# Optimization experiments

Hardware: AMD Instinct MI355X
Metric: run time of the kernel (lower is better)

Reference implementation:

```python
import jax, jax.numpy as jnp
import numpy as np
from jax import lax

N, T, U, V = 32, 512, 100, 4096
BLANK = 0


def setup_inputs() -> dict:
    key = jax.random.key(0)
    k1, k2, k3, k4, k5 = jax.random.split(key, 5)
    encoder_out = jax.random.normal(k1, (N, T, V), dtype=jnp.float32)
    decoder_out = jax.random.normal(k2, (N, U + 1, V), dtype=jnp.float32)
    targets = jax.random.randint(k3, (N, U), 1, V)            # labels, never blank
    input_lengths = jax.random.randint(k4, (N,), T // 2, T + 1)
    target_lengths = jax.random.randint(k5, (N,), U // 2, U + 1)
    return {
        "encoder_out": encoder_out,
        "decoder_out": decoder_out,
        "targets": targets,
        "input_lengths": input_lengths,
        "target_lengths": target_lengths,
    }


def _logprob_single(enc, dec, y, in_len, tgt_len):
    # enc: (T, V)  dec: (U+1, V)  y: (U,)
    Um = y.shape[0]
    u_idx = jnp.arange(Um)
    # emit[t, u] = enc[t, y[u]] + dec[u, y[u]]  (cost of emitting label u+1 at time t)
    emit = enc[:, y] + dec[u_idx, y][None, :]          # (T, U)
    blank_e = enc[:, BLANK]                            # (T,)
    blank_d = dec[:, BLANK]                            # (U+1,)

    # t = 0 row: alpha[0, u] = sum_{k<u} emit[0, k]
    alpha0 = jnp.concatenate([jnp.zeros((1,), enc.dtype), jnp.cumsum(emit[0])])

    def row_step(alpha_prev, xs):
        be_prev, emit_t = xs
        # blank transition from row t-1 (same u)
        top = alpha_prev + be_prev + blank_d           # (U+1,)

        # label transition within row: alpha[u] = logaddexp(top[u], alpha[u-1] + emit_t[u-1])
        def u_step(carry, x):
            top_u, em = x
            a = jnp.logaddexp(top_u, carry + em)
            return a, a

        _, rest = lax.scan(u_step, top[0], (top[1:], emit_t))
        alpha = jnp.concatenate([top[:1], rest])
        return alpha, alpha

    _, rows = lax.scan(row_step, alpha0, (blank_e[:-1], emit[1:]))
    alphas = jnp.concatenate([alpha0[None, :], rows], axis=0)   # (T, U+1)

    # log p(y|x) = alpha[T-1, U] + enc[T-1, blank] + dec[U, blank] with true lengths
    return alphas[in_len - 1, tgt_len] + enc[in_len - 1, BLANK] + dec[tgt_len, BLANK]


def reference(encoder_out, decoder_out, targets, input_lengths, target_lengths):
    # reduction='none': returns per-utterance log p(y|x), shape (N,)
    return jax.vmap(_logprob_single)(encoder_out, decoder_out, targets,
                                     input_lengths, target_lengths)
```

## Files before the change

### kernel.cpp

```cpp
#include <hip/hip_runtime.h>

#define NB 32
#define TT 512
#define UU 100
#define UM 101
#define VV 4096
#define NEG (-1e30f)
#define WIN 64
#define L2E 1.4426950408889634f
#define LN2 0.6931471805599453f

__device__ __forceinline__ float vexp2(float x){ float r; asm("v_exp_f32 %0, %1" : "=v"(r) : "v"(x)); return r; }
__device__ __forceinline__ float vlog2(float x){ float r; asm("v_log_f32 %0, %1" : "=v"(r) : "v"(x)); return r; }

__device__ __forceinline__ float lae2(float a, float b) {
    float m  = fmaxf(a, b);
    float nd = fminf(a, b) - m;
    return m + vlog2(1.0f + vexp2(nd));
}

__global__ __launch_bounds__(1024, 1) void fused_k(
        const float* __restrict__ enc, const float* __restrict__ dec,
        const int* __restrict__ tgt, const int* __restrict__ ilen,
        const int* __restrict__ tlen, float* __restrict__ out) {
    __shared__ float em[2][WIN][128];
    __shared__ float blkL[864];
    __shared__ int   tgtL[UU];
    __shared__ float dvxL[UU];

    int n = blockIdx.x;
    int tid = threadIdx.x;
    int tin = ilen[n], tg = tlen[n];
    int dend = tin - 1 + tg;
    int E = (dend + WIN - 1) / WIN;
    const float* encn = enc + (size_t)n * TT * VV;

    for (int i = tid; i < 864; i += 1024)
        blkL[i] = (i >= 128 && i < 128 + TT) ? encn[(size_t)(i - 128) * VV] * L2E : NEG;
    if (tid < UU) {
        int y = tgt[n * UU + tid];
        tgtL[tid] = y;
        dvxL[tid] = dec[((size_t)n * UM + tid) * VV + y] * L2E;
    }
    __syncthreads();

    int wave = tid >> 6;
    int lane = tid & 63;

    auto FILLWIN = [&](int w, int baseDp) {
        int pid = tid - 64;
        float* emw = &em[w][0][0];
#pragma unroll
        for (int it = 0; it < 9; ++it) {
            int idx = pid + it * 960;
            if (idx < WIN * 128) {
                int dm = idx >> 7, u = idx & 127;
                int d = baseDp + dm + 1;
                int t = d - u;
                float val = NEG;
                if (u >= 1 && u <= tg && t >= 0 && t < tin)
                    val = fmaf(encn[(size_t)t * VV + tgtL[u - 1]], L2E, dvxL[u - 1]);
                emw[idx] = val;
            }
        }
    };

    if (wave != 0) FILLWIN(0, 0);

    int u0c = min(2 * lane, UM - 1), u1c = min(2 * lane + 1, UM - 1);
    float bd0 = dec[((size_t)n * UM + u0c) * VV] * L2E;
    float bd1 = dec[((size_t)n * UM + u1c) * VV] * L2E;
    int ib0 = 127 - 2 * lane;
    bool cap0 = (2 * lane == tg), cap1 = (2 * lane + 1 == tg);
    bool fx16 = (lane == 16), fx32 = (lane == 32), fx48 = (lane == 48);
    float a0 = (lane == 0) ? 0.0f : NEG;
    float a1 = NEG;
    float res = NEG;

    float Ae0[8], Ae1[8], Ab0[8], Ab1[8], Be0[8], Be1[8], Bb0[8], Bb1[8];

    auto REFILL = [&](float (&Re0)[8], float (&Re1)[8], float (&Rb0)[8], float (&Rb1)[8],
                      int j0, int dbase, const float* emb) {
#pragma unroll
        for (int k = 0; k < 8; ++k) {
            int dm = j0 + k;
            float2 ev = *(const float2*)(emb + dm * 128 + 2 * lane);
            int d = dbase + dm + 1;
            Re0[k] = ev.x; Re1[k] = ev.y;
            Rb0[k] = blkL[ib0 + d] + bd0;
            Rb1[k] = blkL[ib0 + d - 1] + bd1;
        }
        __builtin_amdgcn_sched_barrier(0);
    };

    auto STEPS = [&](float (&Re0)[8], float (&Re1)[8], float (&Rb0)[8], float (&Rb1)[8],
                     int j0, int dbase) {
#pragma unroll
        for (int k = 0; k < 8; ++k) {
            int dd = dbase + j0 + k + 1;
            int sh = __builtin_amdgcn_update_dpp(__float_as_int(NEG), __float_as_int(a1),
                                                 0x111, 0xF, 0xF, false);
            float s15 = __int_as_float(__builtin_amdgcn_readlane(__float_as_int(a1), 15));
            float s31 = __int_as_float(__builtin_amdgcn_readlane(__float_as_int(a1), 31));
            float s47 = __int_as_float(__builtin_amdgcn_readlane(__float_as_int(a1), 47));
            float l0 = __int_as_float(sh);
            l0 = fx16 ? s15 : l0;
            l0 = fx32 ? s31 : l0;
            l0 = fx48 ? s47 : l0;
            float bt0 = a0 + Rb0[k], et0 = l0 + Re0[k];
            float bt1 = a1 + Rb1[k], et1 = a0 + Re1[k];
            a0 = lae2(bt0, et0);
            a1 = lae2(bt1, et1);
            if (dd == dend) { if (cap0) res = a0; if (cap1) res = a1; }
        }
        __builtin_amdgcn_sched_barrier(0);
    };

    __syncthreads();

    for (int e = 0; e < E; ++e) {
        if (wave == 0) {
            int dbase = e * WIN;
            const float* emb = &em[e & 1][0][0];
            REFILL(Ae0, Ae1, Ab0, Ab1, 0, dbase, emb);
            REFILL(Be0, Be1, Bb0, Bb1, 8, dbase, emb);  STEPS(Ae0, Ae1, Ab0, Ab1, 0, dbase);
            REFILL(Ae0, Ae1, Ab0, Ab1, 16, dbase, emb); STEPS(Be0, Be1, Bb0, Bb1, 8, dbase);
            REFILL(Be0, Be1, Bb0, Bb1, 24, dbase, emb); STEPS(Ae0, Ae1, Ab0, Ab1, 16, dbase);
            REFILL(Ae0, Ae1, Ab0, Ab1, 32, dbase, emb); STEPS(Be0, Be1, Bb0, Bb1, 24, dbase);
            REFILL(Be0, Be1, Bb0, Bb1, 40, dbase, emb); STEPS(Ae0, Ae1, Ab0, Ab1, 32, dbase);
            REFILL(Ae0, Ae1, Ab0, Ab1, 48, dbase, emb); STEPS(Be0, Be1, Bb0, Bb1, 40, dbase);
            REFILL(Be0, Be1, Bb0, Bb1, 56, dbase, emb); STEPS(Ae0, Ae1, Ab0, Ab1, 48, dbase);
            STEPS(Be0, Be1, Bb0, Bb1, 56, dbase);
        } else {
            FILLWIN((e + 1) & 1, (e + 1) * WIN);
        }
        __syncthreads();
    }

    if (wave == 0 && (cap0 | cap1)) {
        float fin  = blkL[128 + tin - 1];
        float bdtg = dec[((size_t)n * UM + tg) * VV] * L2E;
        out[n] = (res + fin + bdtg) * LN2;
    }
}

extern "C" void kernel_launch(void* const* d_in, const int* in_sizes, int n_in,
                              void* d_out, int out_size, void* d_ws, size_t ws_size,
                              hipStream_t hs) {
    const float* enc  = (const float*)d_in[0];
    const float* dec  = (const float*)d_in[1];
    const int*   tgt  = (const int*)d_in[2];
    const int*   ilen = (const int*)d_in[3];
    const int*   tlen = (const int*)d_in[4];
    float* out = (float*)d_out;

    hipLaunchKernelGGL(fused_k, dim3(NB), dim3(1024), 0, hs,
                       enc, dec, tgt, ilen, tlen, out);
}
```

Before: 71.90 us.

## Replace block barriers with LDS ring buffer and flag-based producer/consumer sync

Swaps the double-buffered window plus __syncthreads handoff between the compute wave and the 15 loader waves for a 4-slot LDS ring. The slots are coordinated by per-slot completion counters and a consumer progress counter, with waits done by spinning and s_sleep. The window shrinks from 64 to 32 diagonals and the row pitch from 128 to 104, so loaders can run several windows ahead and the serial DP wave no longer stalls at block-wide barriers. The cost is spin-wait overhead and a dependence on LDS memory ordering through fences and atomics, which could hide subtle races.

New measurement: 71.81 us. No clear change (-0.1%).

```diff
diff --git a/kernel.cpp b/kernel.cpp
--- a/kernel.cpp
+++ b/kernel.cpp
@@ -6,7 +6,10 @@
 #define UM 101
 #define VV 4096
 #define NEG (-1e30f)
-#define WIN 64
+#define WIN 32
+#define RING 4
+#define PITCH 104
+#define EMSLOT (WIN * PITCH + 24)
 #define L2E 1.4426950408889634f
 #define LN2 0.6931471805599453f
 
@@ -23,53 +26,67 @@
         const float* __restrict__ enc, const float* __restrict__ dec,
         const int* __restrict__ tgt, const int* __restrict__ ilen,
         const int* __restrict__ tlen, float* __restrict__ out) {
-    __shared__ float em[2][WIN][128];
+    __shared__ float emL[RING][EMSLOT];
     __shared__ float blkL[864];
+    __shared__ float dvxL[UU];
     __shared__ int   tgtL[UU];
-    __shared__ float dvxL[UU];
+    __shared__ int   fin[RING];
+    __shared__ int   cons;
 
-    int n = blockIdx.x;
-    int tid = threadIdx.x;
+    int n = blockIdx.x, tid = threadIdx.x;
     int tin = ilen[n], tg = tlen[n];
     int dend = tin - 1 + tg;
     int E = (dend + WIN - 1) / WIN;
     const float* encn = enc + (size_t)n * TT * VV;
+    const float* decn = dec + (size_t)n * UM * VV;
 
     for (int i = tid; i < 864; i += 1024)
         blkL[i] = (i >= 128 && i < 128 + TT) ? encn[(size_t)(i - 128) * VV] * L2E : NEG;
     if (tid < UU) {
         int y = tgt[n * UU + tid];
         tgtL[tid] = y;
-        dvxL[tid] = dec[((size_t)n * UM + tid) * VV + y] * L2E;
+        dvxL[tid] = decn[(size_t)tid * VV + y] * L2E;
     }
+    if (tid < RING) fin[tid] = 0;
+    if (tid == RING) cons = 0;
     __syncthreads();
 
-    int wave = tid >> 6;
-    int lane = tid & 63;
+    int wave = tid >> 6, lane = tid & 63;
 
-    auto FILLWIN = [&](int w, int baseDp) {
-        int pid = tid - 64;
-        float* emw = &em[w][0][0];
+    if (wave != 0) {
+        int cbase = (wave - 1) * 64 + lane;
+        for (int w = 0; w < E; ++w) {
+            int s = w & (RING - 1);
+            while (*(volatile int*)&cons + RING <= w) __builtin_amdgcn_s_sleep(2);
+            float ev[4]; bool ok[4]; int dmA[4], uA[4];
 #pragma unroll
-        for (int it = 0; it < 9; ++it) {
-            int idx = pid + it * 960;
-            if (idx < WIN * 128) {
-                int dm = idx >> 7, u = idx & 127;
-                int d = baseDp + dm + 1;
-                int t = d - u;
-                float val = NEG;
-                if (u >= 1 && u <= tg && t >= 0 && t < tin)
-                    val = fmaf(encn[(size_t)t * VV + tgtL[u - 1]], L2E, dvxL[u - 1]);
-                emw[idx] = val;
+            for (int it = 0; it < 4; ++it) {
+                int c = cbase + it * 960;
+                int dm = (unsigned)c / PITCH;
+                int u  = c - dm * PITCH;
+                int d  = w * WIN + 1 + dm;
+                int t  = d - u;
+                bool v = (c < WIN * PITCH) & (u >= 1) & (u <= tg) & (t >= 0) & (t < tin);
+                dmA[it] = dm; uA[it] = u; ok[it] = v;
+                ev[it] = NEG;
+                if (v) ev[it] = encn[(size_t)t * VV + tgtL[u - 1]];
             }
+#pragma unroll
+            for (int it = 0; it < 4; ++it) {
+                int c = cbase + it * 960;
+                if (c < WIN * PITCH) {
+                    float e = ok[it] ? fmaf(ev[it], L2E, dvxL[uA[it] - 1]) : NEG;
+                    emL[s][dmA[it] * PITCH + uA[it]] = e;
+                }
+            }
+            __threadfence_block();
+            if (lane == 0) atomicAdd(&fin[s], 1);
         }
-    };
+        return;
+    }
 
-    if (wave != 0) FILLWIN(0, 0);
-
-    int u0c = min(2 * lane, UM - 1), u1c = min(2 * lane + 1, UM - 1);
-    float bd0 = dec[((size_t)n * UM + u0c) * VV] * L2E;
-    float bd1 = dec[((size_t)n * UM + u1c) * VV] * L2E;
+    float bd0 = decn[(size_t)min(2 * lane, UM - 1) * VV] * L2E;
+    float bd1 = decn[(size_t)min(2 * lane + 1, UM - 1) * VV] * L2E;
     int ib0 = 127 - 2 * lane;
     bool cap0 = (2 * lane == tg), cap1 = (2 * lane + 1 == tg);
     bool fx16 = (lane == 16), fx32 = (lane == 32), fx48 = (lane == 48);
@@ -79,25 +96,24 @@
 
     float Ae0[8], Ae1[8], Ab0[8], Ab1[8], Be0[8], Be1[8], Bb0[8], Bb1[8];
 
-    auto REFILL = [&](float (&Re0)[8], float (&Re1)[8], float (&Rb0)[8], float (&Rb1)[8],
-                      int j0, int dbase, const float* emb) {
+    auto REFILL = [&](float (&e0)[8], float (&e1)[8], float (&b0)[8], float (&b1)[8],
+                      const float* emb, int j0, int base) {
 #pragma unroll
         for (int k = 0; k < 8; ++k) {
-            int dm = j0 + k;
-            float2 ev = *(const float2*)(emb + dm * 128 + 2 * lane);
-            int d = dbase + dm + 1;
-            Re0[k] = ev.x; Re1[k] = ev.y;
-            Rb0[k] = blkL[ib0 + d] + bd0;
-            Rb1[k] = blkL[ib0 + d - 1] + bd1;
+            int dm = j0 + k, d = base + 1 + dm;
+            float2 ev = *(const float2*)(emb + dm * PITCH + 2 * lane);
+            e0[k] = ev.x; e1[k] = ev.y;
+            b0[k] = blkL[ib0 + d] + bd0;
+            b1[k] = blkL[ib0 + d - 1] + bd1;
         }
         __builtin_amdgcn_sched_barrier(0);
     };
 
-    auto STEPS = [&](float (&Re0)[8], float (&Re1)[8], float (&Rb0)[8], float (&Rb1)[8],
-                     int j0, int dbase) {
+    auto STEPS = [&](float (&e0)[8], float (&e1)[8], float (&b0)[8], float (&b1)[8],
+                     int j0, int base) {
 #pragma unroll
         for (int k = 0; k < 8; ++k) {
-            int dd = dbase + j0 + k + 1;
+            int dd = base + 1 + j0 + k;
             int sh = __builtin_amdgcn_update_dpp(__float_as_int(NEG), __float_as_int(a1),
                                                  0x111, 0xF, 0xF, false);
             float s15 = __int_as_float(__builtin_amdgcn_readlane(__float_as_int(a1), 15));
@@ -107,8 +123,8 @@
             l0 = fx16 ? s15 : l0;
             l0 = fx32 ? s31 : l0;
             l0 = fx48 ? s47 : l0;
-            float bt0 = a0 + Rb0[k], et0 = l0 + Re0[k];
-            float bt1 = a1 + Rb1[k], et1 = a0 + Re1[k];
+            float bt0 = a0 + b0[k], et0 = l0 + e0[k];
+            float bt1 = a1 + b1[k], et1 = a0 + e1[k];
             a0 = lae2(bt0, et0);
             a1 = lae2(bt1, et1);
             if (dd == dend) { if (cap0) res = a0; if (cap1) res = a1; }
@@ -116,31 +132,30 @@
         __builtin_amdgcn_sched_barrier(0);
     };
 
-    __syncthreads();
-
-    for (int e = 0; e < E; ++e) {
-        if (wave == 0) {
-            int dbase = e * WIN;
-            const float* emb = &em[e & 1][0][0];
-            REFILL(Ae0, Ae1, Ab0, Ab1, 0, dbase, emb);
-            REFILL(Be0, Be1, Bb0, Bb1, 8, dbase, emb);  STEPS(Ae0, Ae1, Ab0, Ab1, 0, dbase);
-            REFILL(Ae0, Ae1, Ab0, Ab1, 16, dbase, emb); STEPS(Be0, Be1, Bb0, Bb1, 8, dbase);
-            REFILL(Be0, Be1, Bb0, Bb1, 24, dbase, emb); STEPS(Ae0, Ae1, Ab0, Ab1, 16, dbase);
-            REFILL(Ae0, Ae1, Ab0, Ab1, 32, dbase, emb); STEPS(Be0, Be1, Bb0, Bb1, 24, dbase);
-            REFILL(Be0, Be1, Bb0, Bb1, 40, dbase, emb); STEPS(Ae0, Ae1, Ab0, Ab1, 32, dbase);
-            REFILL(Ae0, Ae1, Ab0, Ab1, 48, dbase, emb); STEPS(Be0, Be1, Bb0, Bb1, 40, dbase);
-            REFILL(Be0, Be1, Bb0, Bb1, 56, dbase, emb); STEPS(Ae0, Ae1, Ab0, Ab1, 48, dbase);
-            STEPS(Be0, Be1, Bb0, Bb1, 56, dbase);
-        } else {
-            FILLWIN((e + 1) & 1, (e + 1) * WIN);
+    for (int w = 0; w < E; ++w) {
+        int s = w & (RING - 1);
+        while (*(volatile int*)&fin[s] < 15) __builtin_amdgcn_s_sleep(2);
+        int base = w * WIN;
+        const float* emb = emL[s];
+        REFILL(Ae0, Ae1, Ab0, Ab1, emb, 0, base);
+        REFILL(Be0, Be1, Bb0, Bb1, emb, 8, base);
+        STEPS(Ae0, Ae1, Ab0, Ab1, 0, base);
+        REFILL(Ae0, Ae1, Ab0, Ab1, emb, 16, base);
+        STEPS(Be0, Be1, Bb0, Bb1, 8, base);
+        REFILL(Be0, Be1, Bb0, Bb1, emb, 24, base);
+        STEPS(Ae0, Ae1, Ab0, Ab1, 16, base);
+        STEPS(Be0, Be1, Bb0, Bb1, 24, base);
+        __threadfence_block();
+        if (lane == 0) {
+            atomicExch(&fin[s], 0);
+            atomicExch(&cons, w + 1);
         }
-        __syncthreads();
     }
 
-    if (wave == 0 && (cap0 | cap1)) {
-        float fin  = blkL[128 + tin - 1];
-        float bdtg = dec[((size_t)n * UM + tg) * VV] * L2E;
-        out[n] = (res + fin + bdtg) * LN2;
+    if (cap0 | cap1) {
+        float fin_  = blkL[128 + tin - 1];
+        float bdtg = decn[(size_t)tg * VV] * L2E;
+        out[n] = (res + fin_ + bdtg) * LN2;
     }
 }
 
```
